# Performance work log

Hardware: AMD Instinct MI355X
Metric: run time of the kernel (lower is better)

The kernel has to match this reference:

```python
import jax, jax.numpy as jnp
import numpy as np

N_NODES = 50000
N_EDGES = 800000
NUM_FEATURES = 256
HIDDEN = 256
HEADS = 8
OUT_DIM = 2


def setup_inputs() -> dict:
    key = jax.random.key(0)
    ks = jax.random.split(key, 16)
    C1 = HIDDEN // HEADS  # 32 per-head channels
    inp = {
        'x': jax.random.normal(ks[0], (N_NODES, NUM_FEATURES), dtype=jnp.float32),
        'edge_index': jax.random.randint(ks[1], (2, N_EDGES), 0, N_NODES, dtype=jnp.int64),
        # layer 1: num_features -> heads * (hidden//heads)
        'W1': jax.random.normal(ks[2], (NUM_FEATURES, HEADS * C1), dtype=jnp.float32) * 0.05,
        'att_src1': jax.random.normal(ks[3], (HEADS, C1), dtype=jnp.float32) * 0.1,
        'att_dst1': jax.random.normal(ks[4], (HEADS, C1), dtype=jnp.float32) * 0.1,
        'b1': jnp.zeros((HEADS * C1,), dtype=jnp.float32),
        # layer 2: hidden -> heads * (hidden//heads)
        'W2': jax.random.normal(ks[5], (HIDDEN, HEADS * C1), dtype=jnp.float32) * 0.05,
        'att_src2': jax.random.normal(ks[6], (HEADS, C1), dtype=jnp.float32) * 0.1,
        'att_dst2': jax.random.normal(ks[7], (HEADS, C1), dtype=jnp.float32) * 0.1,
        'b2': jnp.zeros((HEADS * C1,), dtype=jnp.float32),
        # layer 3: hidden -> output_dim, heads=1, concat=False
        'W3': jax.random.normal(ks[8], (HIDDEN, OUT_DIM), dtype=jnp.float32) * 0.05,
        'att_src3': jax.random.normal(ks[9], (1, OUT_DIM), dtype=jnp.float32) * 0.1,
        'att_dst3': jax.random.normal(ks[10], (1, OUT_DIM), dtype=jnp.float32) * 0.1,
        'b3': jnp.zeros((OUT_DIM,), dtype=jnp.float32),
    }
    return inp


def _gat_layer(x, src, dst, W, a_src, a_dst, b, concat):
    # PyG GATConv: h = x W -> [N, H, C]; e_ij = leaky_relu(a_src.h_j + a_dst.h_i)
    # softmax over edges grouped by destination, then scatter-add h_j * alpha.
    N = x.shape[0]
    H, C = a_src.shape
    h = (x @ W).reshape(N, H, C)
    alpha_s = jnp.einsum('nhc,hc->nh', h, a_src)  # [N, H]
    alpha_d = jnp.einsum('nhc,hc->nh', h, a_dst)
    e = jax.nn.leaky_relu(alpha_s[src] + alpha_d[dst], negative_slope=0.2)  # [E, H]
    m = jax.ops.segment_max(e, dst, num_segments=N)  # per-dst max for stable softmax
    ee = jnp.exp(e - m[dst])
    denom = jax.ops.segment_sum(ee, dst, num_segments=N)
    alpha = ee / (denom[dst] + 1e-16)  # [E, H]
    msg = h[src] * alpha[:, :, None]  # [E, H, C]
    out = jax.ops.segment_sum(msg, dst, num_segments=N)  # [N, H, C]
    out = out.reshape(N, H * C) if concat else out.mean(axis=1)
    return out + b


def reference(x, edge_index, W1, att_src1, att_dst1, b1, W2, att_src2, att_dst2, b2, W3, att_src3, att_dst3, b3):
    N = x.shape[0]
    loops = jnp.arange(N, dtype=edge_index.dtype)
    src = jnp.concatenate([edge_index[0], loops])  # PyG add_self_loops=True
    dst = jnp.concatenate([edge_index[1], loops])
    h = _gat_layer(x, src, dst, W1, att_src1, att_dst1, b1, concat=True)
    h = jax.nn.elu(h)  # dropout is identity in eval mode
    h = _gat_layer(h, src, dst, W2, att_src2, att_dst2, b2, concat=True)
    h = jax.nn.elu(h)
    out = _gat_layer(h, src, dst, W3, att_src3, att_dst3, b3, concat=False)
    return out  # [N, output_dim]; batch=None so pooling/MLP head is skipped
```

## Files before the change

kernel.cpp:

```cpp
#include <hip/hip_runtime.h>
#include <math.h>

#define NF 256
#define NHEADS 8
#define MNEG -1e30f

typedef _Float16 half8 __attribute__((ext_vector_type(8)));
typedef float f32x4 __attribute__((ext_vector_type(4)));


__global__ __launch_bounds__(256) void deg_count_k(const int* __restrict__ dst, int* __restrict__ deg, int E) {
    int e = blockIdx.x * 256 + threadIdx.x;
    if (e < E) atomicAdd(&deg[dst[e]], 1);
}

__global__ __launch_bounds__(256) void scan1_k(const int* __restrict__ deg, int* __restrict__ indptr,
                                               int* __restrict__ bsum, int n) {
    __shared__ int sh[256];
    int tid = threadIdx.x;
    int i = blockIdx.x * 256 + tid;
    int d = (i < n) ? deg[i] : 0;
    sh[tid] = d;
    __syncthreads();
#pragma unroll
    for (int off = 1; off < 256; off <<= 1) {
        int t = (tid >= off) ? sh[tid - off] : 0;
        __syncthreads();
        sh[tid] += t;
        __syncthreads();
    }
    if (i < n) indptr[i] = sh[tid] - d;
    if (tid == 255) bsum[blockIdx.x] = sh[255];
}

__global__ __launch_bounds__(256) void scan3_k(const int* __restrict__ deg, int* __restrict__ indptr,
                                               const int* __restrict__ bsum, int* __restrict__ cursor,
                                               int* __restrict__ srcs, int n, int nb) {
    __shared__ int sh[256];
    int tid = threadIdx.x;
    int d = (tid < nb) ? bsum[tid] : 0;
    sh[tid] = d;
    __syncthreads();
#pragma unroll
    for (int off = 1; off < 256; off <<= 1) {
        int t = (tid >= off) ? sh[tid - off] : 0;
        __syncthreads();
        sh[tid] += t;
        __syncthreads();
    }
    int bid = blockIdx.x;
    int boff = sh[bid] - ((bid < nb) ? bsum[bid] : 0);
    int i = bid * 256 + tid;
    if (i < n) {
        int v = indptr[i] + boff + i;
        indptr[i] = v;
        srcs[v] = i;
        cursor[i] = v + 1;
        if (i == n - 1) indptr[n] = v + deg[i] + 1;
    }
}

__global__ __launch_bounds__(256) void fill_edge_k(const int* __restrict__ esrc, const int* __restrict__ edst,
                                                   int* __restrict__ cursor, int* __restrict__ srcs, int E) {
    int e = blockIdx.x * 256 + threadIdx.x;
    if (e < E) {
        int p = atomicAdd(&cursor[edst[e]], 1);
        srcs[p] = esrc[e];
    }
}


__global__ __launch_bounds__(256) void prep_w_k(const float* __restrict__ W1, const float* __restrict__ W2,
                                                _Float16* __restrict__ O1, _Float16* __restrict__ O2) {
    int tid = blockIdx.x * 256 + threadIdx.x;
    const float* W = (tid < 65536) ? W1 : W2;
    _Float16* O = (tid < 65536) ? O1 : O2;
    int t = tid & 65535;
    int k = t >> 8, c = t & 255;
    O[(size_t)c * 256 + k] = (_Float16)W[t];
}


template <int AF32>
__global__ __launch_bounds__(512, 4) void gemm_mfma_k(const void* __restrict__ Av, const _Float16* __restrict__ WTh,
                                                      const float* __restrict__ att_s, const float* __restrict__ att_d,
                                                      _Float16* __restrict__ C, float* __restrict__ aS,
                                                      float* __restrict__ aD, int M) {
    __shared__ __align__(16) _Float16 Asub[128][72];
    __shared__ __align__(16) _Float16 Wsub[256][72];
    int t = threadIdx.x;
    int wave = t >> 6, lane = t & 63;
    int wm = wave >> 2, wn = wave & 3;
    int lr = lane & 15, lg = lane >> 4;
    int r0 = blockIdx.x * 128;
    const float* Af = (const float*)Av;
    const _Float16* Ah = (const _Float16*)Av;

    int arow = t >> 2;
    int akoff = (t & 3) * 16;
    int wcol = t >> 1;
    int wkoff = (t & 1) * 32;
    int ga_row = r0 + arow; ga_row = ga_row < M ? ga_row : M - 1;

    f32x4 acc[4][4];
#pragma unroll
    for (int mr = 0; mr < 4; ++mr)
#pragma unroll
        for (int nr = 0; nr < 4; ++nr) acc[mr][nr] = (f32x4){0.f, 0.f, 0.f, 0.f};

    for (int ks = 0; ks < 4; ++ks) {
        int k0 = ks * 64;
        __syncthreads();
        if (AF32) {
            const float* p = Af + (size_t)ga_row * 256 + k0 + akoff;
            float4 x0 = *(const float4*)p;
            float4 x1 = *(const float4*)(p + 4);
            float4 x2 = *(const float4*)(p + 8);
            float4 x3 = *(const float4*)(p + 12);
            half8 h0, h1;
            h0[0] = (_Float16)x0.x; h0[1] = (_Float16)x0.y; h0[2] = (_Float16)x0.z; h0[3] = (_Float16)x0.w;
            h0[4] = (_Float16)x1.x; h0[5] = (_Float16)x1.y; h0[6] = (_Float16)x1.z; h0[7] = (_Float16)x1.w;
            h1[0] = (_Float16)x2.x; h1[1] = (_Float16)x2.y; h1[2] = (_Float16)x2.z; h1[3] = (_Float16)x2.w;
            h1[4] = (_Float16)x3.x; h1[5] = (_Float16)x3.y; h1[6] = (_Float16)x3.z; h1[7] = (_Float16)x3.w;
            *(half8*)&Asub[arow][akoff] = h0;
            *(half8*)&Asub[arow][akoff + 8] = h1;
        } else {
            const _Float16* p = Ah + (size_t)ga_row * 256 + k0 + akoff;
            *(half8*)&Asub[arow][akoff] = *(const half8*)p;
            *(half8*)&Asub[arow][akoff + 8] = *(const half8*)(p + 8);
        }
        {
            const _Float16* p = WTh + (size_t)wcol * 256 + k0 + wkoff;
            *(half8*)&Wsub[wcol][wkoff]      = *(const half8*)p;
            *(half8*)&Wsub[wcol][wkoff + 8]  = *(const half8*)(p + 8);
            *(half8*)&Wsub[wcol][wkoff + 16] = *(const half8*)(p + 16);
            *(half8*)&Wsub[wcol][wkoff + 24] = *(const half8*)(p + 24);
        }
        __syncthreads();
#pragma unroll
        for (int kk = 0; kk < 2; ++kk) {
            half8 a[4], b[4];
#pragma unroll
            for (int mr = 0; mr < 4; ++mr)
                a[mr] = *(const half8*)&Asub[wm * 64 + mr * 16 + lr][kk * 32 + lg * 8];
#pragma unroll
            for (int nr = 0; nr < 4; ++nr)
                b[nr] = *(const half8*)&Wsub[wn * 64 + nr * 16 + lr][kk * 32 + lg * 8];
#pragma unroll
            for (int mr = 0; mr < 4; ++mr)
#pragma unroll
                for (int nr = 0; nr < 4; ++nr)
                    acc[mr][nr] = __builtin_amdgcn_mfma_f32_16x16x32_f16(a[mr], b[nr], acc[mr][nr], 0, 0, 0);
        }
    }

    int c0 = wn * 64;
    int h0 = wn * 2, h1 = wn * 2 + 1;
    float as_c0 = att_s[h0 * 32 + lr],      as_c1 = att_s[h0 * 32 + 16 + lr];
    float as_c2 = att_s[h1 * 32 + lr],      as_c3 = att_s[h1 * 32 + 16 + lr];
    float ad_c0 = att_d[h0 * 32 + lr],      ad_c1 = att_d[h0 * 32 + 16 + lr];
    float ad_c2 = att_d[h1 * 32 + lr],      ad_c3 = att_d[h1 * 32 + 16 + lr];

#pragma unroll
    for (int mr = 0; mr < 4; ++mr) {
        int rbase = r0 + wm * 64 + mr * 16 + lg * 4;
#pragma unroll
        for (int j = 0; j < 4; ++j) {
            int row = rbase + j;
            float ps0 = acc[mr][0][j] * as_c0 + acc[mr][1][j] * as_c1;
            float ps1 = acc[mr][2][j] * as_c2 + acc[mr][3][j] * as_c3;
            float pd0 = acc[mr][0][j] * ad_c0 + acc[mr][1][j] * ad_c1;
            float pd1 = acc[mr][2][j] * ad_c2 + acc[mr][3][j] * ad_c3;
#pragma unroll
            for (int o = 1; o < 16; o <<= 1) {
                ps0 += __shfl_xor(ps0, o);
                ps1 += __shfl_xor(ps1, o);
                pd0 += __shfl_xor(pd0, o);
                pd1 += __shfl_xor(pd1, o);
            }
            if (row < M) {
#pragma unroll
                for (int nr = 0; nr < 4; ++nr)
                    C[(size_t)row * 256 + c0 + nr * 16 + lr] = (_Float16)acc[mr][nr][j];
                if (lr == 0) {
                    aS[(size_t)row * NHEADS + h0] = ps0;
                    aS[(size_t)row * NHEADS + h1] = ps1;
                    aD[(size_t)row * NHEADS + h0] = pd0;
                    aD[(size_t)row * NHEADS + h1] = pd1;
                }
            }
        }
    }
}


template <int MODE>
__global__ __launch_bounds__(256) void agg_k(const _Float16* __restrict__ h, const float* __restrict__ aS,
                                             const float* __restrict__ aD, const int* __restrict__ indptr,
                                             const int* __restrict__ srcs, const float* __restrict__ bias,
                                             _Float16* __restrict__ out,
                                             const float* __restrict__ W3, const float* __restrict__ as3,
                                             const float* __restrict__ ad3, float* __restrict__ h3,
                                             float* __restrict__ s3, float* __restrict__ d3, int N) {
    int wid = blockIdx.x * 4 + (threadIdx.x >> 6);
    if (wid >= N) return;
    int lane = threadIdx.x & 63;
    int hf = lane >> 5;
    int cl = lane & 31;
    int hh = cl >> 2;
    float ad = aD[(size_t)wid * NHEADS + hh];
    int beg = indptr[wid], end = indptr[wid + 1];
    const half8* h8p = (const half8*)h;
    float m = MNEG, den = 0.f;
    float f0 = 0, f1 = 0, f2 = 0, f3 = 0, f4 = 0, f5 = 0, f6 = 0, f7 = 0;
    int k = beg;
    int sp[4];
    if (k + 8 <= end) {
#pragma unroll
        for (int j = 0; j < 4; ++j) sp[j] = srcs[k + 2 * j + hf];
    }
    for (; k + 8 <= end; k += 8) {
        int s[4]; float as[4]; half8 v[4]; float e[4];
#pragma unroll
        for (int j = 0; j < 4; ++j) s[j] = sp[j];
        if (k + 16 <= end) {
#pragma unroll
            for (int j = 0; j < 4; ++j) sp[j] = srcs[k + 8 + 2 * j + hf];
        }
#pragma unroll
        for (int j = 0; j < 4; ++j) as[j] = aS[(size_t)s[j] * NHEADS + hh];
#pragma unroll
        for (int j = 0; j < 4; ++j) v[j] = h8p[(size_t)s[j] * 32 + cl];
#pragma unroll
        for (int j = 0; j < 4; ++j) { e[j] = as[j] + ad; e[j] = fmaxf(e[j], 0.2f * e[j]); }
        float em = fmaxf(fmaxf(e[0], e[1]), fmaxf(e[2], e[3]));
        if (__any(em > m + 4.f)) {
            float mn = fmaxf(m, em);
            float sc = __expf(m - mn);
            den *= sc; f0 *= sc; f1 *= sc; f2 *= sc; f3 *= sc; f4 *= sc; f5 *= sc; f6 *= sc; f7 *= sc;
            m = mn;
        }
        half8 hacc = (half8)(_Float16)0.f;
#pragma unroll
        for (int j = 0; j < 4; ++j) {
            float p = __expf(e[j] - m);
            den += p;
            _Float16 ph = (_Float16)p;
            half8 pb = {ph, ph, ph, ph, ph, ph, ph, ph};
            hacc += v[j] * pb;
        }
        f0 += (float)hacc[0]; f1 += (float)hacc[1]; f2 += (float)hacc[2]; f3 += (float)hacc[3];
        f4 += (float)hacc[4]; f5 += (float)hacc[5]; f6 += (float)hacc[6]; f7 += (float)hacc[7];
    }
    for (; k + 2 <= end; k += 2) {
        int s = srcs[k + hf];
        float as = aS[(size_t)s * NHEADS + hh];
        half8 v = h8p[(size_t)s * 32 + cl];
        float e = as + ad; e = fmaxf(e, 0.2f * e);
        if (__any(e > m + 4.f)) {
            float mn = fmaxf(m, e);
            float sc = __expf(m - mn);
            den *= sc; f0 *= sc; f1 *= sc; f2 *= sc; f3 *= sc; f4 *= sc; f5 *= sc; f6 *= sc; f7 *= sc;
            m = mn;
        }
        float p = __expf(e - m);
        den += p;
        f0 += p * (float)v[0]; f1 += p * (float)v[1]; f2 += p * (float)v[2]; f3 += p * (float)v[3];
        f4 += p * (float)v[4]; f5 += p * (float)v[5]; f6 += p * (float)v[6]; f7 += p * (float)v[7];
    }
    if (k < end) {
        int s = srcs[k];
        float e = aS[(size_t)s * NHEADS + hh] + ad;
        e = fmaxf(e, 0.2f * e);
        half8 v = h8p[(size_t)s * 32 + cl];
        float eg = (hf == 0) ? e : MNEG;
        if (__any(eg > m + 4.f)) {
            float mn = fmaxf(m, eg);
            float sc = __expf(m - mn);
            den *= sc; f0 *= sc; f1 *= sc; f2 *= sc; f3 *= sc; f4 *= sc; f5 *= sc; f6 *= sc; f7 *= sc;
            m = mn;
        }
        float p = (hf == 0) ? __expf(e - m) : 0.f;
        den += p;
        f0 += p * (float)v[0]; f1 += p * (float)v[1]; f2 += p * (float)v[2]; f3 += p * (float)v[3];
        f4 += p * (float)v[4]; f5 += p * (float)v[5]; f6 += p * (float)v[6]; f7 += p * (float)v[7];
    }
    {
        float m2 = __shfl_xor(m, 32);
        float den2 = __shfl_xor(den, 32);
        float mn = fmaxf(m, m2);
        float sc1 = __expf(m - mn), sc2 = __expf(m2 - mn);
        den = den * sc1 + den2 * sc2;
        f0 = f0 * sc1 + __shfl_xor(f0, 32) * sc2;
        f1 = f1 * sc1 + __shfl_xor(f1, 32) * sc2;
        f2 = f2 * sc1 + __shfl_xor(f2, 32) * sc2;
        f3 = f3 * sc1 + __shfl_xor(f3, 32) * sc2;
        f4 = f4 * sc1 + __shfl_xor(f4, 32) * sc2;
        f5 = f5 * sc1 + __shfl_xor(f5, 32) * sc2;
        f6 = f6 * sc1 + __shfl_xor(f6, 32) * sc2;
        f7 = f7 * sc1 + __shfl_xor(f7, 32) * sc2;
    }
    float inv = 1.f / (den + 1e-16f);
    float4 bv0 = *(const float4*)&bias[cl * 8];
    float4 bv1 = *(const float4*)&bias[cl * 8 + 4];
    float o[8];
    o[0] = f0 * inv + bv0.x; o[1] = f1 * inv + bv0.y; o[2] = f2 * inv + bv0.z; o[3] = f3 * inv + bv0.w;
    o[4] = f4 * inv + bv1.x; o[5] = f5 * inv + bv1.y; o[6] = f6 * inv + bv1.z; o[7] = f7 * inv + bv1.w;
#pragma unroll
    for (int c = 0; c < 8; ++c) o[c] = (o[c] > 0.f) ? o[c] : expm1f(o[c]);

    if (MODE == 0) {
        if (hf == 0) {
            half8 ov;
#pragma unroll
            for (int c = 0; c < 8; ++c) ov[c] = (_Float16)o[c];
            ((half8*)out)[(size_t)wid * 32 + cl] = ov;
        }
    } else {
        const float4* W34 = (const float4*)W3;
        float p0 = 0.f, p1 = 0.f;
#pragma unroll
        for (int q = 0; q < 4; ++q) {
            float4 w = W34[cl * 4 + q];
            p0 += o[2 * q] * w.x + o[2 * q + 1] * w.z;
            p1 += o[2 * q] * w.y + o[2 * q + 1] * w.w;
        }
#pragma unroll
        for (int off = 1; off < 32; off <<= 1) {
            p0 += __shfl_xor(p0, off);
            p1 += __shfl_xor(p1, off);
        }
        if (lane == 0) {
            h3[(size_t)wid * 2] = p0;
            h3[(size_t)wid * 2 + 1] = p1;
            s3[wid] = p0 * as3[0] + p1 * as3[1];
            d3[wid] = p0 * ad3[0] + p1 * ad3[1];
        }
    }
}


__global__ __launch_bounds__(256) void agg3_k(const float* __restrict__ h3, const float* __restrict__ s3,
                                              const float* __restrict__ d3, const int* __restrict__ indptr,
                                              const int* __restrict__ srcs, const float* __restrict__ b3,
                                              float* __restrict__ out, int N) {
    int t = blockIdx.x * 256 + threadIdx.x;
    int n = t >> 2;
    if (n >= N) return;
    int sub = t & 3;
    float ad = d3[n];
    float m = MNEG, den = 0.f, a0 = 0.f, a1 = 0.f;
    int beg = indptr[n], end = indptr[n + 1];
    for (int k = beg + sub; k < end; k += 4) {
        int s = srcs[k];
        float e = s3[s] + ad;
        e = fmaxf(e, 0.2f * e);
        if (e > m + 8.f) {
            float mn = fmaxf(m, e);
            float sc = __expf(m - mn);
            den *= sc; a0 *= sc; a1 *= sc;
            m = mn;
        }
        float p = __expf(e - m);
        den += p;
        a0 += p * h3[(size_t)s * 2];
        a1 += p * h3[(size_t)s * 2 + 1];
    }
#pragma unroll
    for (int off = 1; off < 4; off <<= 1) {
        float m2 = __shfl_xor(m, off);
        float den2 = __shfl_xor(den, off);
        float a02 = __shfl_xor(a0, off);
        float a12 = __shfl_xor(a1, off);
        float mn = fmaxf(m, m2);
        float sc1 = __expf(m - mn);
        float sc2 = __expf(m2 - mn);
        den = den * sc1 + den2 * sc2;
        a0 = a0 * sc1 + a02 * sc2;
        a1 = a1 * sc1 + a12 * sc2;
        m = mn;
    }
    if (sub == 0) {
        float inv = 1.f / (den + 1e-16f);
        out[(size_t)n * 2]     = a0 * inv + b3[0];
        out[(size_t)n * 2 + 1] = a1 * inv + b3[1];
    }
}


extern "C" void kernel_launch(void* const* d_in, const int* in_sizes, int n_in,
                              void* d_out, int out_size, void* d_ws, size_t ws_size,
                              hipStream_t stream) {
    const float* x   = (const float*)d_in[0];
    const int*   ei  = (const int*)d_in[1];
    const float* W1  = (const float*)d_in[2];
    const float* as1 = (const float*)d_in[3];
    const float* ad1 = (const float*)d_in[4];
    const float* b1  = (const float*)d_in[5];
    const float* W2  = (const float*)d_in[6];
    const float* as2 = (const float*)d_in[7];
    const float* ad2 = (const float*)d_in[8];
    const float* b2  = (const float*)d_in[9];
    const float* W3  = (const float*)d_in[10];
    const float* at_s3 = (const float*)d_in[11];
    const float* at_d3 = (const float*)d_in[12];
    const float* b3  = (const float*)d_in[13];

    int N = in_sizes[0] / NF;
    int E = in_sizes[1] / 2;
    const int* esrc = ei;
    const int* edst = ei + E;

    char* w = (char*)d_ws;
    _Float16* hbuf  = (_Float16*)w; w += (size_t)N * NF * 2;
    _Float16* xnext = (_Float16*)w; w += (size_t)N * NF * 2;
    float* aS    = (float*)w; w += (size_t)N * NHEADS * 4;
    float* aD    = (float*)w; w += (size_t)N * NHEADS * 4;
    float* h3    = (float*)w; w += (size_t)N * 2 * 4;
    float* s3    = (float*)w; w += (size_t)N * 4;
    float* d3    = (float*)w; w += (size_t)N * 4;
    int* deg     = (int*)w; w += (size_t)N * 4;
    int* indptr  = (int*)w; w += (size_t)(N + 1) * 4 + 60;
    int* cursor  = (int*)w; w += (size_t)N * 4;
    int* bsum    = (int*)w; w += 256 * 4;
    _Float16* WTh1 = (_Float16*)w; w += (size_t)256 * 256 * 2;
    _Float16* WTh2 = (_Float16*)w; w += (size_t)256 * 256 * 2;
    int* srcs    = (int*)w;

    int nb_n = (N + 255) / 256;
    int nb_e = (E + 255) / 256;
    int nb_w = (N + 3) / 4;
    int nb_gm = (N + 127) / 128;
    int nb_a3 = (N * 4 + 255) / 256;

    hipMemsetAsync(deg, 0, (size_t)N * 4, stream);
    deg_count_k<<<nb_e, 256, 0, stream>>>(edst, deg, E);
    scan1_k<<<nb_n, 256, 0, stream>>>(deg, indptr, bsum, N);
    scan3_k<<<nb_n, 256, 0, stream>>>(deg, indptr, bsum, cursor, srcs, N, nb_n);
    fill_edge_k<<<nb_e, 256, 0, stream>>>(esrc, edst, cursor, srcs, E);
    prep_w_k<<<512, 256, 0, stream>>>(W1, W2, WTh1, WTh2);

    gemm_mfma_k<1><<<nb_gm, 512, 0, stream>>>(x, WTh1, as1, ad1, hbuf, aS, aD, N);
    agg_k<0><<<nb_w, 256, 0, stream>>>(hbuf, aS, aD, indptr, srcs, b1, xnext,
                                       nullptr, nullptr, nullptr, nullptr, nullptr, nullptr, N);
    gemm_mfma_k<0><<<nb_gm, 512, 0, stream>>>(xnext, WTh2, as2, ad2, hbuf, aS, aD, N);
    agg_k<1><<<nb_w, 256, 0, stream>>>(hbuf, aS, aD, indptr, srcs, b2, nullptr,
                                       W3, at_s3, at_d3, h3, s3, d3, N);
    agg3_k<<<nb_a3, 256, 0, stream>>>(h3, s3, d3, indptr, srcs, b3, (float*)d_out, N);
}
```

Baseline: 300.7 us.

## Double-buffer GEMM LDS tiles with register prefetch and vectorize edge atomics

The MFMA GEMM now uses two LDS buffers with a K-step of 32 instead of one buffer with a K-step of 64. It prefetches the next tile's global loads into registers while MFMAs run on the current tile, so global latency overlaps with compute. The CSR build kernels (degree count and edge fill) now have each thread handle four edges through int4 loads, which cuts the thread count. The trade-off is that the GEMM runs twice as many K iterations, each with two barriers, and register pressure rises.

```diff
diff --git a/kernel.cpp b/kernel.cpp
--- a/kernel.cpp
+++ b/kernel.cpp
@@ -10,8 +10,16 @@
 
 
 __global__ __launch_bounds__(256) void deg_count_k(const int* __restrict__ dst, int* __restrict__ deg, int E) {
-    int e = blockIdx.x * 256 + threadIdx.x;
-    if (e < E) atomicAdd(&deg[dst[e]], 1);
+    int i = (blockIdx.x * 256 + threadIdx.x) * 4;
+    if (i + 4 <= E) {
+        int4 d = *(const int4*)&dst[i];
+        atomicAdd(&deg[d.x], 1);
+        atomicAdd(&deg[d.y], 1);
+        atomicAdd(&deg[d.z], 1);
+        atomicAdd(&deg[d.w], 1);
+    } else {
+        for (int e = i; e < E; ++e) atomicAdd(&deg[dst[e]], 1);
+    }
 }
 
 __global__ __launch_bounds__(256) void scan1_k(const int* __restrict__ deg, int* __restrict__ indptr,
@@ -62,10 +70,16 @@
 
 __global__ __launch_bounds__(256) void fill_edge_k(const int* __restrict__ esrc, const int* __restrict__ edst,
                                                    int* __restrict__ cursor, int* __restrict__ srcs, int E) {
-    int e = blockIdx.x * 256 + threadIdx.x;
-    if (e < E) {
-        int p = atomicAdd(&cursor[edst[e]], 1);
-        srcs[p] = esrc[e];
+    int i = (blockIdx.x * 256 + threadIdx.x) * 4;
+    if (i + 4 <= E) {
+        int4 s = *(const int4*)&esrc[i];
+        int4 d = *(const int4*)&edst[i];
+        srcs[atomicAdd(&cursor[d.x], 1)] = s.x;
+        srcs[atomicAdd(&cursor[d.y], 1)] = s.y;
+        srcs[atomicAdd(&cursor[d.z], 1)] = s.z;
+        srcs[atomicAdd(&cursor[d.w], 1)] = s.w;
+    } else {
+        for (int e = i; e < E; ++e) srcs[atomicAdd(&cursor[edst[e]], 1)] = esrc[e];
     }
 }
 
@@ -86,8 +100,8 @@
                                                       const float* __restrict__ att_s, const float* __restrict__ att_d,
                                                       _Float16* __restrict__ C, float* __restrict__ aS,
                                                       float* __restrict__ aD, int M) {
-    __shared__ __align__(16) _Float16 Asub[128][72];
-    __shared__ __align__(16) _Float16 Wsub[256][72];
+    __shared__ __align__(16) _Float16 Asub[2][128][40];
+    __shared__ __align__(16) _Float16 Wsub[2][256][40];
     int t = threadIdx.x;
     int wave = t >> 6, lane = t & 63;
     int wm = wave >> 2, wn = wave & 3;
@@ -96,61 +110,74 @@
     const float* Af = (const float*)Av;
     const _Float16* Ah = (const _Float16*)Av;
 
-    int arow = t >> 2;
-    int akoff = (t & 3) * 16;
-    int wcol = t >> 1;
-    int wkoff = (t & 1) * 32;
+    int arow = t >> 2, aoff = (t & 3) * 8;
+    int wcol = t >> 1, woff = (t & 1) * 16;
     int ga_row = r0 + arow; ga_row = ga_row < M ? ga_row : M - 1;
 
-    f32x4 acc[4][4];
-#pragma unroll
-    for (int mr = 0; mr < 4; ++mr)
-#pragma unroll
-        for (int nr = 0; nr < 4; ++nr) acc[mr][nr] = (f32x4){0.f, 0.f, 0.f, 0.f};
-
-    for (int ks = 0; ks < 4; ++ks) {
-        int k0 = ks * 64;
-        __syncthreads();
+    half8 aR, wR0, wR1;
+    {
         if (AF32) {
-            const float* p = Af + (size_t)ga_row * 256 + k0 + akoff;
+            const float* p = Af + (size_t)ga_row * 256 + aoff;
             float4 x0 = *(const float4*)p;
             float4 x1 = *(const float4*)(p + 4);
-            float4 x2 = *(const float4*)(p + 8);
-            float4 x3 = *(const float4*)(p + 12);
-            half8 h0, h1;
-            h0[0] = (_Float16)x0.x; h0[1] = (_Float16)x0.y; h0[2] = (_Float16)x0.z; h0[3] = (_Float16)x0.w;
-            h0[4] = (_Float16)x1.x; h0[5] = (_Float16)x1.y; h0[6] = (_Float16)x1.z; h0[7] = (_Float16)x1.w;
-            h1[0] = (_Float16)x2.x; h1[1] = (_Float16)x2.y; h1[2] = (_Float16)x2.z; h1[3] = (_Float16)x2.w;
-            h1[4] = (_Float16)x3.x; h1[5] = (_Float16)x3.y; h1[6] = (_Float16)x3.z; h1[7] = (_Float16)x3.w;
-            *(half8*)&Asub[arow][akoff] = h0;
-            *(half8*)&Asub[arow][akoff + 8] = h1;
+            aR[0] = (_Float16)x0.x; aR[1] = (_Float16)x0.y; aR[2] = (_Float16)x0.z; aR[3] = (_Float16)x0.w;
+            aR[4] = (_Float16)x1.x; aR[5] = (_Float16)x1.y; aR[6] = (_Float16)x1.z; aR[7] = (_Float16)x1.w;
         } else {
-            const _Float16* p = Ah + (size_t)ga_row * 256 + k0 + akoff;
-            *(half8*)&Asub[arow][akoff] = *(const half8*)p;
-            *(half8*)&Asub[arow][akoff + 8] = *(const half8*)(p + 8);
+            aR = *(const half8*)(Ah + (size_t)ga_row * 256 + aoff);
+        }
+        const _Float16* p = WTh + (size_t)wcol * 256 + woff;
+        wR0 = *(const half8*)p;
+        wR1 = *(const half8*)(p + 8);
+    }
+    *(half8*)&Asub[0][arow][aoff] = aR;
+    *(half8*)&Wsub[0][wcol][woff] = wR0;
+    *(half8*)&Wsub[0][wcol][woff + 8] = wR1;
+    __syncthreads();
+
+    f32x4 acc[4][4];
+#pragma unroll
+    for (int mr = 0; mr < 4; ++mr)
+#pragma unroll
+        for (int nr = 0; nr < 4; ++nr) acc[mr][nr] = (f32x4){0.f, 0.f, 0.f, 0.f};
+
+#pragma unroll
+    for (int ks = 0; ks < 8; ++ks) {
+        int cur = ks & 1;
+        if (ks < 7) {
+            int k0 = (ks + 1) * 32;
+            if (AF32) {
+                const float* p = Af + (size_t)ga_row * 256 + k0 + aoff;
+                float4 x0 = *(const float4*)p;
+                float4 x1 = *(const float4*)(p + 4);
+                aR[0] = (_Float16)x0.x; aR[1] = (_Float16)x0.y; aR[2] = (_Float16)x0.z; aR[3] = (_Float16)x0.w;
+                aR[4] = (_Float16)x1.x; aR[5] = (_Float16)x1.y; aR[6] = (_Float16)x1.z; aR[7] = (_Float16)x1.w;
+            } else {
+                aR = *(const half8*)(Ah + (size_t)ga_row * 256 + k0 + aoff);
+            }
+            const _Float16* p = WTh + (size_t)wcol * 256 + k0 + woff;
+            wR0 = *(const half8*)p;
+            wR1 = *(const half8*)(p + 8);
         }
         {
-            const _Float16* p = WTh + (size_t)wcol * 256 + k0 + wkoff;
-            *(half8*)&Wsub[wcol][wkoff]      = *(const half8*)p;
-            *(half8*)&Wsub[wcol][wkoff + 8]  = *(const half8*)(p + 8);
-            *(half8*)&Wsub[wcol][wkoff + 16] = *(const half8*)(p + 16);
-            *(half8*)&Wsub[wcol][wkoff + 24] = *(const half8*)(p + 24);
-        }
-        __syncthreads();
-#pragma unroll
-        for (int kk = 0; kk < 2; ++kk) {
             half8 a[4], b[4];
 #pragma unroll
             for (int mr = 0; mr < 4; ++mr)
-                a[mr] = *(const half8*)&Asub[wm * 64 + mr * 16 + lr][kk * 32 + lg * 8];
+                a[mr] = *(const half8*)&Asub[cur][wm * 64 + mr * 16 + lr][lg * 8];
 #pragma unroll
             for (int nr = 0; nr < 4; ++nr)
-                b[nr] = *(const half8*)&Wsub[wn * 64 + nr * 16 + lr][kk * 32 + lg * 8];
+                b[nr] = *(const half8*)&Wsub[cur][wn * 64 + nr * 16 + lr][lg * 8];
 #pragma unroll
             for (int mr = 0; mr < 4; ++mr)
 #pragma unroll
                 for (int nr = 0; nr < 4; ++nr)
                     acc[mr][nr] = __builtin_amdgcn_mfma_f32_16x16x32_f16(a[mr], b[nr], acc[mr][nr], 0, 0, 0);
+        }
+        if (ks < 7) {
+            __syncthreads();
+            *(half8*)&Asub[cur ^ 1][arow][aoff] = aR;
+            *(half8*)&Wsub[cur ^ 1][wcol][woff] = wR0;
+            *(half8*)&Wsub[cur ^ 1][wcol][woff + 8] = wR1;
+            __syncthreads();
         }
     }
 
@@ -428,16 +455,16 @@
     int* srcs    = (int*)w;
 
     int nb_n = (N + 255) / 256;
-    int nb_e = (E + 255) / 256;
+    int nb_e4 = (E + 1023) / 1024;
     int nb_w = (N + 3) / 4;
     int nb_gm = (N + 127) / 128;
     int nb_a3 = (N * 4 + 255) / 256;
 
     hipMemsetAsync(deg, 0, (size_t)N * 4, stream);
-    deg_count_k<<<nb_e, 256, 0, stream>>>(edst, deg, E);
+    deg_count_k<<<nb_e4, 256, 0, stream>>>(edst, deg, E);
     scan1_k<<<nb_n, 256, 0, stream>>>(deg, indptr, bsum, N);
     scan3_k<<<nb_n, 256, 0, stream>>>(deg, indptr, bsum, cursor, srcs, N, nb_n);
-    fill_edge_k<<<nb_e, 256, 0, stream>>>(esrc, edst, cursor, srcs, E);
+    fill_edge_k<<<nb_e4, 256, 0, stream>>>(esrc, edst, cursor, srcs, E);
     prep_w_k<<<512, 256, 0, stream>>>(W1, W2, WTh1, WTh2);
 
     gemm_mfma_k<1><<<nb_gm, 512, 0, stream>>>(x, WTh1, as1, ad1, hbuf, aS, aD, N);
```

Result: faster. 293.5 us (-2.4%).
